# Kernel tuning notes

Measured on AMD Instinct MI355X. Metric: run time of the kernel, lower is better.

Reference implementation:

```python
import jax, jax.numpy as jnp
import numpy as np

B, N, D, H, F = 2, 2048, 1024, 16, 4096
HD = D // H


def setup_inputs() -> dict:
    key = jax.random.key(0)
    ks = jax.random.split(key, 16)
    s = 0.02
    x = jax.random.normal(ks[0], (B, N, D), jnp.float32)
    # tail padding: lengths in [N//2, N]; position >= length is padded
    lengths = jax.random.randint(ks[1], (B,), N // 2, N + 1)
    key_padding_mask = jnp.arange(N)[None, :] >= lengths[:, None]  # [B,N] bool, True = pad
    return {
        "x": x,
        "key_padding_mask": key_padding_mask,
        "ln1_g": jnp.ones((D,), jnp.float32),
        "ln1_b": jnp.zeros((D,), jnp.float32),
        "w_in": jax.random.normal(ks[2], (3 * D, D), jnp.float32) * s,  # packed QKV in_proj
        "b_in": jnp.zeros((3 * D,), jnp.float32),
        "w_out": jax.random.normal(ks[3], (D, D), jnp.float32) * s,
        "b_out": jnp.zeros((D,), jnp.float32),
        "ln2_g": jnp.ones((D,), jnp.float32),
        "ln2_b": jnp.zeros((D,), jnp.float32),
        "w1": jax.random.normal(ks[4], (F, D), jnp.float32) * s,
        "b1": jnp.zeros((F,), jnp.float32),
        "w2": jax.random.normal(ks[5], (D, F), jnp.float32) * s,
        "b2": jnp.zeros((D,), jnp.float32),
    }


def _layernorm(x, g, b):
    # source LayerNorm forces fp32 then casts back
    xf = x.astype(jnp.float32)
    m = xf.mean(-1, keepdims=True)
    v = xf.var(-1, keepdims=True)
    return (((xf - m) * jax.lax.rsqrt(v + 1e-5)) * g + b).astype(x.dtype)


def _quick_gelu(x):
    return x * jax.nn.sigmoid(1.702 * x)


def _block(x, key_padding_mask, ln1_g, ln1_b, w_in, b_in, w_out, b_out,
           ln2_g, ln2_b, w1, b1, w2, b2):
    n = x.shape[1]
    # combined mask: causal OR key-pad, with diagonal unmasked for padded query rows
    causal = jnp.triu(jnp.ones((n, n), bool), 1)                      # [N,N]
    combined = causal[None] | key_padding_mask[:, None, :]            # [B,N,N]
    diag = jnp.eye(n, dtype=bool)
    combined = combined & ~(diag[None] & key_padding_mask[:, :, None])

    # --- attention (pre-norm) ---
    xn = _layernorm(x, ln1_g, ln1_b)
    qkv = xn @ w_in.T + b_in                                          # [B,N,3D]
    q, k, v = jnp.split(qkv, 3, axis=-1)
    def heads(t):
        return t.reshape(x.shape[0], n, H, HD).transpose(0, 2, 1, 3)  # [B,H,N,hd]
    q, k, v = heads(q), heads(k), heads(v)
    scores = jnp.einsum('bhqd,bhkd->bhqk', q, k) / np.sqrt(HD)        # [B,H,N,N]
    scores = jnp.where(combined[:, None], -jnp.inf, scores)
    probs = jax.nn.softmax(scores, axis=-1)                           # [B,H,N,N]
    attn = jnp.einsum('bhqk,bhkd->bqhd', probs, v).reshape(x.shape[0], n, D)
    attn = attn @ w_out.T + b_out
    attn = jnp.where(key_padding_mask[:, :, None], 0.0, attn)         # zero padded queries
    weights = probs.mean(axis=1)                                      # need_weights avg over heads

    x = x + attn
    # --- FFN (pre-norm) ---
    xn = _layernorm(x, ln2_g, ln2_b)
    mlp = _quick_gelu(xn @ w1.T + b1) @ w2.T + b2
    x = x + mlp
    return x, weights


def reference(x, key_padding_mask, ln1_g, ln1_b, w_in, b_in, w_out, b_out,
              ln2_g, ln2_b, w1, b1, w2, b2):
    return _block(x, key_padding_mask, ln1_g, ln1_b, w_in, b_in, w_out, b_out,
                  ln2_g, ln2_b, w1, b1, w2, b2)
```

## Files before the change

kernel.cpp:

```cpp
#include <hip/hip_runtime.h>
#include <hip/hip_bf16.h>
#include <stdint.h>

#define DEVI __device__ __forceinline__

typedef __attribute__((ext_vector_type(8)))  short bf16x8;
typedef __attribute__((ext_vector_type(4)))  short s16x4;
typedef __attribute__((ext_vector_type(4)))  float f32x4;
typedef __attribute__((ext_vector_type(16))) float f32x16;
typedef __attribute__((ext_vector_type(2)))  unsigned int u32x2;
typedef __attribute__((ext_vector_type(4)))  unsigned int u32x4;

#define L2E 1.44269504088896f

DEVI unsigned short f2bf(float f){
  union{float f; unsigned int u;} v; v.f = f;
  unsigned int u = v.u;
  u = u + 0x7FFFu + ((u >> 16) & 1u);
  return (unsigned short)(u >> 16);
}

DEVI unsigned int cvt_pk_bf16(float lo, float hi){
  unsigned int r;
  asm("v_cvt_pk_bf16_f32 %0, %1, %2" : "=v"(r) : "v"(lo), "v"(hi));
  return r;
}

typedef const __attribute__((address_space(1))) unsigned int gq_t;
typedef __attribute__((address_space(3))) unsigned int lq_t;

DEVI void gl_lds16(const unsigned short* g, unsigned short* l){
  __builtin_amdgcn_global_load_lds((gq_t*)(uintptr_t)g, (lq_t*)(uintptr_t)l, 16, 0, 0);
}

__global__ void prep_len(const unsigned char* mask, int* lens){
  __shared__ int nz, cnt0, cnt1;
  int tid = threadIdx.x;
  if(tid == 0){ nz = 0; cnt0 = 0; cnt1 = 0; }
  __syncthreads();
  int loc = 0;
  for(int i = tid; i < 4096; i += 256) loc |= mask[i];
  if(loc) atomicOr(&nz, 1);
  __syncthreads();
  bool isu8 = (nz != 0);
  const int* m32 = (const int*)mask;
  int c0 = 0, c1 = 0;
  for(int i = tid; i < 2048; i += 256){
    int p0 = isu8 ? (int)mask[i]        : m32[i];
    int p1 = isu8 ? (int)mask[2048 + i] : m32[2048 + i];
    c0 += (p0 == 0);
    c1 += (p1 == 0);
  }
  atomicAdd(&cnt0, c0);
  atomicAdd(&cnt1, c1);
  __syncthreads();
  if(tid == 0){ lens[0] = cnt0; lens[1] = cnt1; }
}

__global__ void conv_bf16(const float* s, unsigned short* d, int n4){
  int i = blockIdx.x * 256 + threadIdx.x;
  if(i >= n4) return;
  f32x4 v = *(const f32x4*)(s + (size_t)i*4);
  s16x4 o;
  o[0]=(short)f2bf(v[0]); o[1]=(short)f2bf(v[1]);
  o[2]=(short)f2bf(v[2]); o[3]=(short)f2bf(v[3]);
  *(s16x4*)(d + (size_t)i*4) = o;
}

__global__ __launch_bounds__(256)
void ln_k(const float* x, const float* g, const float* b, unsigned short* y){
  int row = blockIdx.x, tid = threadIdx.x;
  const float* xr = x + (size_t)row*1024;
  f32x4 v = *(const f32x4*)(xr + tid*4);
  float s = v[0]+v[1]+v[2]+v[3];
#pragma unroll
  for(int o=1;o<64;o<<=1) s += __shfl_xor(s, o, 64);
  __shared__ float red[8];
  if((tid & 63) == 0) red[tid>>6] = s;
  __syncthreads();
  float mean = (red[0]+red[1]+red[2]+red[3]) * 0.0009765625f;
  float d0=v[0]-mean, d1=v[1]-mean, d2=v[2]-mean, d3=v[3]-mean;
  float s2 = d0*d0 + d1*d1 + d2*d2 + d3*d3;
#pragma unroll
  for(int o=1;o<64;o<<=1) s2 += __shfl_xor(s2, o, 64);
  if((tid & 63) == 0) red[4 + (tid>>6)] = s2;
  __syncthreads();
  float var = (red[4]+red[5]+red[6]+red[7]) * 0.0009765625f;
  float rstd = rsqrtf(var + 1e-5f);
  f32x4 gg = *(const f32x4*)(g + tid*4);
  f32x4 bb = *(const f32x4*)(b + tid*4);
  s16x4 o;
  o[0] = (short)f2bf(d0*rstd*gg[0] + bb[0]);
  o[1] = (short)f2bf(d1*rstd*gg[1] + bb[1]);
  o[2] = (short)f2bf(d2*rstd*gg[2] + bb[2]);
  o[3] = (short)f2bf(d3*rstd*gg[3] + bb[3]);
  *(s16x4*)(y + (size_t)row*1024 + tid*4) = o;
}

struct GemmP {
  const unsigned short* Wt;
  const unsigned short* Xa;
  int Nmat, K;
  const float* bias;
  const float* resid;
  const int* lens;
  float* outF;
  unsigned short* outB;
};

template<int EPI, int NB>
__global__ __launch_bounds__(256)
void gemm_k(GemmP p){
  constexpr int NF = NB/32;
  __shared__ unsigned short lw[NB*64];
  __shared__ unsigned short lx[128*64];
  int nbn = p.Nmat / NB;
  int id = blockIdx.x;
  int cpx = gridDim.x >> 3;
  id = (id & 7)*cpx + (id >> 3);
  int bm = id / nbn, bn = id % nbn;
  int tid = threadIdx.x, lane = tid & 63, g = lane >> 4, l15 = lane & 15;
  int wave = tid >> 6, wm = wave & 1, wn = wave >> 1;

  const unsigned short* srcW[NB/32]; const unsigned short* srcX[4];
  unsigned short* dstW[NB/32]; unsigned short* dstX[4];
#pragma unroll
  for(int i=0;i<NB/32;++i){
    int slot = i*256 + tid, row = slot >> 3, c = slot & 7, cs = c ^ (row & 7);
    srcW[i] = p.Wt + (size_t)(bn*NB + row)*p.K + cs*8;
    dstW[i] = lw + (i*256 + (tid & 192))*8;
  }
#pragma unroll
  for(int i=0;i<4;++i){
    int slot = i*256 + tid, row = slot >> 3, c = slot & 7, cs = c ^ (row & 7);
    srcX[i] = p.Xa + (size_t)(bm*128 + row)*p.K + cs*8;
    dstX[i] = lx + (i*256 + (tid & 192))*8;
  }

  f32x4 acc[NF][4];
#pragma unroll
  for(int a=0;a<NF;++a)
#pragma unroll
    for(int bb=0;bb<4;++bb)
#pragma unroll
      for(int e=0;e<4;++e) acc[a][bb][e] = 0.f;

  int iters = p.K >> 6;
  for(int kt=0; kt<iters; ++kt){
#pragma unroll
    for(int i=0;i<NB/32;++i){
      gl_lds16(srcW[i], dstW[i]);
      srcW[i] += 64;
    }
#pragma unroll
    for(int i=0;i<4;++i){
      gl_lds16(srcX[i], dstX[i]);
      srcX[i] += 64;
    }
    __syncthreads();
#pragma unroll
    for(int kc=0;kc<2;++kc){
      bf16x8 af[NF], bfr[4];
#pragma unroll
      for(int nf=0;nf<NF;++nf){
        int row = wn*(16*NF) + nf*16 + l15;
        int ch = (kc*4 + g) ^ (row & 7);
        af[nf] = *(const bf16x8*)(lw + row*64 + ch*8);
      }
#pragma unroll
      for(int mf=0;mf<4;++mf){
        int row = wm*64 + mf*16 + l15;
        int ch = (kc*4 + g) ^ (row & 7);
        bfr[mf] = *(const bf16x8*)(lx + row*64 + ch*8);
      }
#pragma unroll
      for(int nf=0;nf<NF;++nf)
#pragma unroll
        for(int mf=0;mf<4;++mf)
          acc[nf][mf] = __builtin_amdgcn_mfma_f32_16x16x32_bf16(af[nf], bfr[mf], acc[nf][mf], 0, 0, 0);
    }
    __syncthreads();
  }

#pragma unroll
  for(int mf=0;mf<4;++mf){
    int m = bm*128 + wm*64 + mf*16 + l15;
#pragma unroll
    for(int nf=0;nf<NF;++nf){
      int n = bn*NB + wn*(16*NF) + nf*16 + g*4;
      f32x4 v = acc[nf][mf];
      f32x4 bz = *(const f32x4*)(p.bias + n);
      v = v + bz;
      if constexpr(EPI == 0){
        float sc = (n < 1024) ? 0.125f : 1.0f;
        s16x4 o;
#pragma unroll
        for(int e=0;e<4;++e) o[e] = (short)f2bf(v[e]*sc);
        *(s16x4*)(p.outB + (size_t)m*p.Nmat + n) = o;
      } else if constexpr(EPI == 1){
        int b_ = m >> 11, q = m & 2047;
        f32x4 r = *(const f32x4*)(p.resid + (size_t)m*1024 + n);
        if(q >= p.lens[b_]){ v[0]=0.f; v[1]=0.f; v[2]=0.f; v[3]=0.f; }
        v = v + r;
        *(f32x4*)(p.outF + (size_t)m*p.Nmat + n) = v;
      } else if constexpr(EPI == 2){
        s16x4 o;
#pragma unroll
        for(int e=0;e<4;++e){
          float sg = v[e]*__builtin_amdgcn_rcpf(1.f + exp2f(-1.702f*L2E*v[e]));
          o[e] = (short)f2bf(sg);
        }
        *(s16x4*)(p.outB + (size_t)m*p.Nmat + n) = o;
      } else {
        f32x4 r = *(const f32x4*)(p.resid + (size_t)m*p.Nmat + n);
        v = v + r;
        *(f32x4*)(p.outF + (size_t)m*p.Nmat + n) = v;
      }
    }
  }
}

__global__ __launch_bounds__(256)
void repack_vt(const unsigned short* qkv, unsigned short* vt){
  __shared__ unsigned short t[64*80];
  int id = blockIdx.x;
  int bh = id >> 5, nt = id & 31;
  int b = bh >> 4, h = bh & 15;
  int tid = threadIdx.x;
  int r = tid >> 2, c0 = (tid & 3)*16;
  const unsigned short* src = qkv + ((size_t)(b*2048 + nt*64 + r)*3072 + 2048 + h*64 + c0);
  bf16x8 v0 = *(const bf16x8*)(src);
  bf16x8 v1 = *(const bf16x8*)(src + 8);
  *(bf16x8*)(t + r*80 + c0) = v0;
  *(bf16x8*)(t + r*80 + c0 + 8) = v1;
  __syncthreads();
#pragma unroll
  for(int cc=0; cc<2; ++cc){
    int ci = cc*256 + tid;
    int hd = ci >> 3, nc = (ci & 7)*8;
    bf16x8 o;
#pragma unroll
    for(int i=0;i<8;++i) o[i] = (short)t[(nc+i)*80 + hd];
    *(bf16x8*)(vt + ((size_t)(bh*64 + hd)*2048 + nt*64 + nc)) = o;
  }
}

__global__ __launch_bounds__(256)
void attn_flash(const unsigned short* qkv, const unsigned short* vt,
                unsigned short* attnO, float* mrow, float* lrow, const int* lens)
{
  __shared__ unsigned short lk[2][64*64];
  __shared__ unsigned short lv[2][64*64];
  int id = blockIdx.x;
  int jj = id & 255;
  int bh = jj & 31;
  int qt = (id < 256) ? (15 - (jj >> 5)) : (jj >> 5);
  int b = bh >> 4, h = bh & 15;
  int tid = threadIdx.x, lane = tid & 63, wave = tid >> 6;
  int hi = lane >> 5, l31 = lane & 31;
  int q = qt*128 + wave*32 + l31;
  int len_b = lens[b];

  const unsigned short* qptr = qkv + ((size_t)(b*2048 + q)*3072 + h*64);
  bf16x8 qf[4];
#pragma unroll
  for(int ks=0;ks<4;++ks) qf[ks] = *(const bf16x8*)(qptr + ks*16 + hi*8);

  const unsigned short* srcK[2]; const unsigned short* srcV[2];
  int dof[2];
#pragma unroll
  for(int i=0;i<2;++i){
    int slot = i*256 + tid, row = slot >> 3, c = slot & 7, cs = c ^ (row & 7);
    srcK[i] = qkv + ((size_t)(b*2048 + row)*3072 + 1024 + h*64) + cs*8;
    srcV[i] = vt + ((size_t)(bh*64 + row)*2048) + cs*8;
    dof[i] = (i*256 + (tid & 192))*8;
  }

  f32x16 oacc[2];
#pragma unroll
  for(int a=0;a<2;++a)
#pragma unroll
    for(int e=0;e<16;++e) oacc[a][e] = 0.f;
  float mcur = -1e30f, lsum = 0.f;
  int ktmax = qt*2 + 1;

#pragma unroll
  for(int i=0;i<2;++i){
    gl_lds16(srcK[i], &lk[0][dof[i]]);
    gl_lds16(srcV[i], &lv[0][dof[i]]);
    srcK[i] += (size_t)64*3072;
    srcV[i] += 64;
  }
  __syncthreads();

  int buf = 0;
  for(int kt=0; kt<=ktmax; ++kt){
    if(kt < ktmax){
#pragma unroll
      for(int i=0;i<2;++i){
        gl_lds16(srcK[i], &lk[buf^1][dof[i]]);
        gl_lds16(srcV[i], &lv[buf^1][dof[i]]);
        srcK[i] += (size_t)64*3072;
        srcV[i] += 64;
      }
    }

    f32x16 s2[2];
#pragma unroll
    for(int kb=0;kb<2;++kb){
      f32x16 a;
#pragma unroll
      for(int e=0;e<16;++e) a[e] = 0.f;
      int row = kb*32 + l31;
#pragma unroll
      for(int ks=0;ks<4;++ks){
        int ch = (ks*2 + hi) ^ (row & 7);
        bf16x8 kf = *(const bf16x8*)(&lk[buf][0] + row*64 + ch*8);
        a = __builtin_amdgcn_mfma_f32_32x32x16_bf16(kf, qf[ks], a, 0, 0, 0);
      }
      s2[kb] = a;
    }

    float tmax = -1e30f;
    bool full = (kt*64 + 63 < qt*128 + wave*32) && (kt*64 + 64 <= len_b);
    if(full){
#pragma unroll
      for(int kb=0;kb<2;++kb)
#pragma unroll
        for(int r=0;r<16;++r){
          float tv = s2[kb][r]*L2E;
          s2[kb][r] = tv;
          tmax = fmaxf(tmax, tv);
        }
    } else {
#pragma unroll
      for(int kb=0;kb<2;++kb)
#pragma unroll
        for(int r=0;r<16;++r){
          int key = kt*64 + kb*32 + (r&3) + 8*(r>>2) + 4*hi;
          bool ok = (key == q) || ((key < q) && (key < len_b));
          float tv = ok ? s2[kb][r]*L2E : -1e30f;
          s2[kb][r] = tv;
          tmax = fmaxf(tmax, tv);
        }
    }
    tmax = fmaxf(tmax, __shfl_xor(tmax, 32, 64));

    if(!__all(tmax <= mcur + 8.f)){
      float mnew = fmaxf(mcur, tmax);
      float fsc = exp2f(mcur - mnew);
      lsum *= fsc;
#pragma unroll
      for(int a=0;a<2;++a)
#pragma unroll
        for(int e=0;e<16;++e) oacc[a][e] *= fsc;
      mcur = mnew;
    }
    float rsum = 0.f;
#pragma unroll
    for(int kb=0;kb<2;++kb)
#pragma unroll
      for(int r=0;r<16;++r){
        float pv = exp2f(s2[kb][r] - mcur);
        s2[kb][r] = pv;
        rsum += pv;
      }
    rsum += __shfl_xor(rsum, 32, 64);
    lsum += rsum;

#pragma unroll
    for(int ks=0;ks<4;++ks){
      int kb = ks >> 1, r0 = (ks & 1)*8;
      unsigned int a0 = cvt_pk_bf16(s2[kb][r0+0], s2[kb][r0+1]);
      unsigned int a1 = cvt_pk_bf16(s2[kb][r0+2], s2[kb][r0+3]);
      unsigned int a2 = cvt_pk_bf16(s2[kb][r0+4], s2[kb][r0+5]);
      unsigned int a3 = cvt_pk_bf16(s2[kb][r0+6], s2[kb][r0+7]);
      unsigned int b0 = __shfl_xor(a0, 32, 64);
      unsigned int b1 = __shfl_xor(a1, 32, 64);
      unsigned int b2 = __shfl_xor(a2, 32, 64);
      unsigned int b3 = __shfl_xor(a3, 32, 64);
      union { u32x4 u; bf16x8 s8; } pw;
      pw.u[0] = hi ? b2 : a0;
      pw.u[1] = hi ? b3 : a1;
      pw.u[2] = hi ? a2 : b0;
      pw.u[3] = hi ? a3 : b1;
#pragma unroll
      for(int af=0;af<2;++af){
        int vrow = af*32 + l31;
        int ch = (ks*2 + hi) ^ (vrow & 7);
        bf16x8 vf = *(const bf16x8*)(&lv[buf][0] + vrow*64 + ch*8);
        oacc[af] = __builtin_amdgcn_mfma_f32_32x32x16_bf16(vf, pw.s8, oacc[af], 0, 0, 0);
      }
    }
    __syncthreads();
    buf ^= 1;
  }

  float rl = __builtin_amdgcn_rcpf(lsum);
  if(hi == 0){
    mrow[(size_t)bh*2048 + q] = mcur;
    lrow[(size_t)bh*2048 + q] = lsum;
  }
  unsigned short* obase = attnO + ((size_t)(b*2048 + q)*1024 + h*64);
#pragma unroll
  for(int af=0;af<2;++af)
#pragma unroll
    for(int grp=0; grp<4; ++grp){
      int hd0 = af*32 + grp*8 + hi*4;
      u32x2 st;
      st[0] = cvt_pk_bf16(oacc[af][grp*4+0]*rl, oacc[af][grp*4+1]*rl);
      st[1] = cvt_pk_bf16(oacc[af][grp*4+2]*rl, oacc[af][grp*4+3]*rl);
      *(u32x2*)(obase + hd0) = st;
    }
}

__global__ void prep_c(const float* mrow, const float* lrow, float* cbuf){
  int i = blockIdx.x*256 + threadIdx.x;
  cbuf[i] = exp2f(-mrow[i]) * __builtin_amdgcn_rcpf(lrow[i]);
}

__global__ __launch_bounds__(256)
void attn_weights(const unsigned short* qkv, const float* cbuf,
                  float* wout, const int* lens)
{
  int id = blockIdx.x;
  int kt = id & 15, qt = (id >> 4) & 15, b = id >> 8;
  int tid = threadIdx.x;
  float* wtile = wout + ((size_t)(b*2048 + qt*128))*2048 + kt*128;

  if(kt > qt){
    f32x4 z; z[0]=0.f; z[1]=0.f; z[2]=0.f; z[3]=0.f;
#pragma unroll
    for(int i=0;i<8;++i){
      float* p = wtile + (size_t)(i*16 + (tid>>4))*2048 + (tid&15)*8;
      *(f32x4*)p = z; *(f32x4*)(p+4) = z;
    }
    return;
  }

  __shared__ unsigned short lk[2][128*64];
  __shared__ unsigned short lq[2][128*64];
  int lane = tid & 63, wave = tid >> 6, hi = lane >> 5, l31 = lane & 31;
  int len_b = lens[b];
  int q_abs = qt*128 + wave*32 + l31;

  const float* cb = cbuf + (size_t)(b*16)*2048 + q_abs;
  float ccs[16];
#pragma unroll
  for(int h=0;h<16;++h) ccs[h] = cb[(size_t)h*2048];

  const unsigned short* srcK[4]; const unsigned short* srcQ[4]; int dA[4];
#pragma unroll
  for(int i=0;i<4;++i){
    int d = i*256 + tid, row = d >> 3, c = d & 7, cs = c ^ (row & 7);
    srcK[i] = qkv + ((size_t)(b*2048 + kt*128 + row)*3072 + 1024) + cs*8;
    srcQ[i] = qkv + ((size_t)(b*2048 + qt*128 + row)*3072) + cs*8;
    dA[i] = d*8;
  }

  float wacc[4][16];
#pragma unroll
  for(int ksub=0;ksub<4;++ksub)
#pragma unroll
    for(int r=0;r<16;++r) wacc[ksub][r] = 0.f;

#pragma unroll
  for(int i=0;i<4;++i){
    gl_lds16(srcK[i], &lk[0][dA[i]]);
    gl_lds16(srcQ[i], &lq[0][dA[i]]);
  }
  __syncthreads();

  int buf = 0;
  for(int h=0;h<16;++h){
    if(h < 15){
#pragma unroll
      for(int i=0;i<4;++i){
        gl_lds16(srcK[i] + (h+1)*64, &lk[buf^1][dA[i]]);
        gl_lds16(srcQ[i] + (h+1)*64, &lq[buf^1][dA[i]]);
      }
    }
    bf16x8 qf[4];
#pragma unroll
    for(int ks=0;ks<4;++ks){
      int row = wave*32 + l31;
      int ch = (ks*2 + hi) ^ (row & 7);
      qf[ks] = *(const bf16x8*)(&lq[buf][0] + row*64 + ch*8);
    }
    float cc = ccs[h];
#pragma unroll
    for(int ksub=0;ksub<4;++ksub){
      f32x16 sc;
#pragma unroll
      for(int e=0;e<16;++e) sc[e] = 0.f;
#pragma unroll
      for(int ks=0;ks<4;++ks){
        int row = ksub*32 + l31;
        int ch = (ks*2 + hi) ^ (row & 7);
        bf16x8 kf = *(const bf16x8*)(&lk[buf][0] + row*64 + ch*8);
        sc = __builtin_amdgcn_mfma_f32_32x32x16_bf16(kf, qf[ks], sc, 0, 0, 0);
      }
#pragma unroll
      for(int r=0;r<16;++r)
        wacc[ksub][r] += exp2f(sc[r]*L2E) * cc;
    }
    __syncthreads();
    buf ^= 1;
  }

#pragma unroll
  for(int ksub=0;ksub<4;++ksub)
#pragma unroll
    for(int rg=0;rg<4;++rg){
      f32x4 v;
#pragma unroll
      for(int e=0;e<4;++e){
        int key_abs = kt*128 + ksub*32 + rg*8 + hi*4 + e;
        bool ok = (key_abs == q_abs) || ((key_abs < q_abs) && (key_abs < len_b));
        v[e] = ok ? wacc[ksub][rg*4 + e]*0.0625f : 0.f;
      }
      *(f32x4*)(wtile + (size_t)(wave*32 + l31)*2048 + ksub*32 + rg*8 + hi*4) = v;
    }
}

extern "C" void kernel_launch(void* const* d_in, const int* in_sizes, int n_in,
                              void* d_out, int out_size, void* d_ws, size_t ws_size,
                              hipStream_t stream)
{
  const float* x     = (const float*)d_in[0];
  const unsigned char* mask = (const unsigned char*)d_in[1];
  const float* ln1g  = (const float*)d_in[2];
  const float* ln1b  = (const float*)d_in[3];
  const float* w_in  = (const float*)d_in[4];
  const float* b_in  = (const float*)d_in[5];
  const float* w_out = (const float*)d_in[6];
  const float* b_out = (const float*)d_in[7];
  const float* ln2g  = (const float*)d_in[8];
  const float* ln2b  = (const float*)d_in[9];
  const float* w1    = (const float*)d_in[10];
  const float* b1    = (const float*)d_in[11];
  const float* w2    = (const float*)d_in[12];
  const float* b2    = (const float*)d_in[13];
  float* out = (float*)d_out;

  char* ws = (char*)d_ws;
  size_t off = 0;
  auto take = [&](size_t bytes)->char*{
    char* p = ws + off; off += (bytes + 255) & ~(size_t)255; return p;
  };
  int* lens            = (int*)take(256);
  unsigned short* wq   = (unsigned short*)take((size_t)3072*1024*2);
  unsigned short* wo   = (unsigned short*)take((size_t)1024*1024*2);
  unsigned short* w1c  = (unsigned short*)take((size_t)4096*1024*2);
  unsigned short* w2c  = (unsigned short*)take((size_t)1024*4096*2);
  unsigned short* xn   = (unsigned short*)take((size_t)4096*1024*2);
  unsigned short* qkv  = (unsigned short*)take((size_t)4096*3072*2);
  unsigned short* vt   = (unsigned short*)take((size_t)32*64*2048*2);
  float* mrow          = (float*)take((size_t)32*2048*4);
  float* lrow          = (float*)take((size_t)32*2048*4);
  float* cbuf          = (float*)take((size_t)32*2048*4);
  unsigned short* aO   = (unsigned short*)take((size_t)4096*1024*2);
  float* x1            = (float*)take((size_t)4096*1024*4);
  unsigned short* hmid = (unsigned short*)take((size_t)4096*4096*2);

  prep_len<<<1,256,0,stream>>>(mask, lens);
  conv_bf16<<<3072,256,0,stream>>>(w_in, wq, 786432);
  conv_bf16<<<1024,256,0,stream>>>(w_out, wo, 262144);
  conv_bf16<<<4096,256,0,stream>>>(w1, w1c, 1048576);
  conv_bf16<<<4096,256,0,stream>>>(w2, w2c, 1048576);
  ln_k<<<4096,256,0,stream>>>(x, ln1g, ln1b, xn);

  GemmP p1{wq, xn, 3072, 1024, b_in, nullptr, nullptr, nullptr, qkv};
  gemm_k<0,128><<<768,256,0,stream>>>(p1);
  repack_vt<<<1024,256,0,stream>>>(qkv, vt);
  attn_flash<<<512,256,0,stream>>>(qkv, vt, aO, mrow, lrow, lens);
  prep_c<<<256,256,0,stream>>>(mrow, lrow, cbuf);
  attn_weights<<<512,256,0,stream>>>(qkv, cbuf, out + 4194304, lens);

  GemmP p2{wo, aO, 1024, 1024, b_out, x, lens, x1, nullptr};
  gemm_k<1,64><<<512,256,0,stream>>>(p2);
  ln_k<<<4096,256,0,stream>>>(x1, ln2g, ln2b, xn);
  GemmP p3{w1c, xn, 4096, 1024, b1, nullptr, nullptr, nullptr, hmid};
  gemm_k<2,128><<<1024,256,0,stream>>>(p3);
  GemmP p4{w2c, hmid, 1024, 4096, b2, x1, nullptr, out, nullptr};
  gemm_k<3,64><<<512,256,0,stream>>>(p4);
}
```

Measured before the change: 338.1 us.

## Triple-buffer attention K/V loads, fold log2e into Q, widen GEMM K-tile

The flash-attention loop moves from double to triple LDS buffering. The two per-iteration __syncthreads are replaced by one explicit vmcnt wait plus a barrier, and MFMA sections get raised wave priority, so global loads overlap compute with fewer stalls. The log2(e) factor is folded into the Q scaling in the QKV GEMM epilogue, which removes a multiply per score in both attention kernels; rounding of Q to bf16 now includes that factor. The GEMM is templated on its K-tile depth, and the two 64-wide-N GEMMs use K=128 to halve loop iterations and barriers, at the cost of more shared memory per block.

```diff
diff --git a/kernel.cpp b/kernel.cpp
--- a/kernel.cpp
+++ b/kernel.cpp
@@ -108,12 +108,15 @@
   unsigned short* outB;
 };
 
-template<int EPI, int NB>
+template<int EPI, int NB, int KB>
 __global__ __launch_bounds__(256)
 void gemm_k(GemmP p){
   constexpr int NF = NB/32;
-  __shared__ unsigned short lw[NB*64];
-  __shared__ unsigned short lx[128*64];
+  constexpr int CPR = KB/8;
+  constexpr int NW = (NB*KB)/2048;
+  constexpr int NX = (128*KB)/2048;
+  __shared__ unsigned short lw[NB*KB];
+  __shared__ unsigned short lx[128*KB];
   int nbn = p.Nmat / NB;
   int id = blockIdx.x;
   int cpx = gridDim.x >> 3;
@@ -122,17 +125,17 @@
   int tid = threadIdx.x, lane = tid & 63, g = lane >> 4, l15 = lane & 15;
   int wave = tid >> 6, wm = wave & 1, wn = wave >> 1;
 
-  const unsigned short* srcW[NB/32]; const unsigned short* srcX[4];
-  unsigned short* dstW[NB/32]; unsigned short* dstX[4];
-#pragma unroll
-  for(int i=0;i<NB/32;++i){
-    int slot = i*256 + tid, row = slot >> 3, c = slot & 7, cs = c ^ (row & 7);
+  const unsigned short* srcW[NW]; const unsigned short* srcX[NX];
+  unsigned short* dstW[NW]; unsigned short* dstX[NX];
+#pragma unroll
+  for(int i=0;i<NW;++i){
+    int slot = i*256 + tid, row = slot/CPR, c = slot%CPR, cs = c ^ (row & 7);
     srcW[i] = p.Wt + (size_t)(bn*NB + row)*p.K + cs*8;
     dstW[i] = lw + (i*256 + (tid & 192))*8;
   }
 #pragma unroll
-  for(int i=0;i<4;++i){
-    int slot = i*256 + tid, row = slot >> 3, c = slot & 7, cs = c ^ (row & 7);
+  for(int i=0;i<NX;++i){
+    int slot = i*256 + tid, row = slot/CPR, c = slot%CPR, cs = c ^ (row & 7);
     srcX[i] = p.Xa + (size_t)(bm*128 + row)*p.K + cs*8;
     dstX[i] = lx + (i*256 + (tid & 192))*8;
   }
@@ -145,33 +148,33 @@
 #pragma unroll
       for(int e=0;e<4;++e) acc[a][bb][e] = 0.f;
 
-  int iters = p.K >> 6;
+  int iters = p.K / KB;
   for(int kt=0; kt<iters; ++kt){
 #pragma unroll
-    for(int i=0;i<NB/32;++i){
+    for(int i=0;i<NW;++i){
       gl_lds16(srcW[i], dstW[i]);
-      srcW[i] += 64;
-    }
-#pragma unroll
-    for(int i=0;i<4;++i){
+      srcW[i] += KB;
+    }
+#pragma unroll
+    for(int i=0;i<NX;++i){
       gl_lds16(srcX[i], dstX[i]);
-      srcX[i] += 64;
+      srcX[i] += KB;
     }
     __syncthreads();
 #pragma unroll
-    for(int kc=0;kc<2;++kc){
+    for(int kc=0;kc<KB/32;++kc){
       bf16x8 af[NF], bfr[4];
 #pragma unroll
       for(int nf=0;nf<NF;++nf){
         int row = wn*(16*NF) + nf*16 + l15;
         int ch = (kc*4 + g) ^ (row & 7);
-        af[nf] = *(const bf16x8*)(lw + row*64 + ch*8);
+        af[nf] = *(const bf16x8*)(lw + row*KB + ch*8);
       }
 #pragma unroll
       for(int mf=0;mf<4;++mf){
         int row = wm*64 + mf*16 + l15;
         int ch = (kc*4 + g) ^ (row & 7);
-        bfr[mf] = *(const bf16x8*)(lx + row*64 + ch*8);
+        bfr[mf] = *(const bf16x8*)(lx + row*KB + ch*8);
       }
 #pragma unroll
       for(int nf=0;nf<NF;++nf)
@@ -192,7 +195,7 @@
       f32x4 bz = *(const f32x4*)(p.bias + n);
       v = v + bz;
       if constexpr(EPI == 0){
-        float sc = (n < 1024) ? 0.125f : 1.0f;
+        float sc = (n < 1024) ? 0.125f*L2E : 1.0f;
         s16x4 o;
 #pragma unroll
         for(int e=0;e<4;++e) o[e] = (short)f2bf(v[e]*sc);
@@ -249,8 +252,8 @@
 void attn_flash(const unsigned short* qkv, const unsigned short* vt,
                 unsigned short* attnO, float* mrow, float* lrow, const int* lens)
 {
-  __shared__ unsigned short lk[2][64*64];
-  __shared__ unsigned short lv[2][64*64];
+  __shared__ unsigned short lk[3][64*64];
+  __shared__ unsigned short lv[3][64*64];
   int id = blockIdx.x;
   int jj = id & 255;
   int bh = jj & 31;
@@ -265,6 +268,7 @@
   bf16x8 qf[4];
 #pragma unroll
   for(int ks=0;ks<4;++ks) qf[ks] = *(const bf16x8*)(qptr + ks*16 + hi*8);
+  asm volatile("" :: "v"(qf[0]), "v"(qf[1]), "v"(qf[2]), "v"(qf[3]), "s"(len_b));
 
   const unsigned short* srcK[2]; const unsigned short* srcV[2];
   int dof[2];
@@ -291,21 +295,26 @@
     srcK[i] += (size_t)64*3072;
     srcV[i] += 64;
   }
-  __syncthreads();
 
   int buf = 0;
   for(int kt=0; kt<=ktmax; ++kt){
+    int nb = buf + 1; if(nb == 3) nb = 0;
     if(kt < ktmax){
 #pragma unroll
       for(int i=0;i<2;++i){
-        gl_lds16(srcK[i], &lk[buf^1][dof[i]]);
-        gl_lds16(srcV[i], &lv[buf^1][dof[i]]);
+        gl_lds16(srcK[i], &lk[nb][dof[i]]);
+        gl_lds16(srcV[i], &lv[nb][dof[i]]);
         srcK[i] += (size_t)64*3072;
         srcV[i] += 64;
       }
-    }
+      asm volatile("s_waitcnt vmcnt(4)" ::: "memory");
+    } else {
+      asm volatile("s_waitcnt vmcnt(0)" ::: "memory");
+    }
+    asm volatile("s_barrier" ::: "memory");
 
     f32x16 s2[2];
+    __builtin_amdgcn_s_setprio(1);
 #pragma unroll
     for(int kb=0;kb<2;++kb){
       f32x16 a;
@@ -320,6 +329,7 @@
       }
       s2[kb] = a;
     }
+    __builtin_amdgcn_s_setprio(0);
 
     float tmax = -1e30f;
     bool full = (kt*64 + 63 < qt*128 + wave*32) && (kt*64 + 64 <= len_b);
@@ -327,11 +337,8 @@
 #pragma unroll
       for(int kb=0;kb<2;++kb)
 #pragma unroll
-        for(int r=0;r<16;++r){
-          float tv = s2[kb][r]*L2E;
-          s2[kb][r] = tv;
-          tmax = fmaxf(tmax, tv);
-        }
+        for(int r=0;r<16;++r)
+          tmax = fmaxf(tmax, s2[kb][r]);
     } else {
 #pragma unroll
       for(int kb=0;kb<2;++kb)
@@ -339,7 +346,7 @@
         for(int r=0;r<16;++r){
           int key = kt*64 + kb*32 + (r&3) + 8*(r>>2) + 4*hi;
           bool ok = (key == q) || ((key < q) && (key < len_b));
-          float tv = ok ? s2[kb][r]*L2E : -1e30f;
+          float tv = ok ? s2[kb][r] : -1e30f;
           s2[kb][r] = tv;
           tmax = fmaxf(tmax, tv);
         }
@@ -368,6 +375,7 @@
     rsum += __shfl_xor(rsum, 32, 64);
     lsum += rsum;
 
+    __builtin_amdgcn_s_setprio(1);
 #pragma unroll
     for(int ks=0;ks<4;++ks){
       int kb = ks >> 1, r0 = (ks & 1)*8;
@@ -392,8 +400,8 @@
         oacc[af] = __builtin_amdgcn_mfma_f32_32x32x16_bf16(vf, pw.s8, oacc[af], 0, 0, 0);
       }
     }
-    __syncthreads();
-    buf ^= 1;
+    __builtin_amdgcn_s_setprio(0);
+    buf = nb;
   }
 
   float rl = __builtin_amdgcn_rcpf(lsum);
@@ -502,7 +510,7 @@
       }
 #pragma unroll
       for(int r=0;r<16;++r)
-        wacc[ksub][r] += exp2f(sc[r]*L2E) * cc;
+        wacc[ksub][r] += exp2f(sc[r]) * cc;
     }
     __syncthreads();
     buf ^= 1;
@@ -571,17 +579,17 @@
   ln_k<<<4096,256,0,stream>>>(x, ln1g, ln1b, xn);
 
   GemmP p1{wq, xn, 3072, 1024, b_in, nullptr, nullptr, nullptr, qkv};
-  gemm_k<0,128><<<768,256,0,stream>>>(p1);
+  gemm_k<0,128,64><<<768,256,0,stream>>>(p1);
   repack_vt<<<1024,256,0,stream>>>(qkv, vt);
   attn_flash<<<512,256,0,stream>>>(qkv, vt, aO, mrow, lrow, lens);
   prep_c<<<256,256,0,stream>>>(mrow, lrow, cbuf);
   attn_weights<<<512,256,0,stream>>>(qkv, cbuf, out + 4194304, lens);
 
   GemmP p2{wo, aO, 1024, 1024, b_out, x, lens, x1, nullptr};
-  gemm_k<1,64><<<512,256,0,stream>>>(p2);
+  gemm_k<1,64,128><<<512,256,0,stream>>>(p2);
   ln_k<<<4096,256,0,stream>>>(x1, ln2g, ln2b, xn);
   GemmP p3{w1c, xn, 4096, 1024, b1, nullptr, nullptr, nullptr, hmid};
-  gemm_k<2,128><<<1024,256,0,stream>>>(p3);
+  gemm_k<2,128,64><<<1024,256,0,stream>>>(p3);
   GemmP p4{w2c, hmid, 1024, 4096, b2, x1, nullptr, out, nullptr};
-  gemm_k<3,64><<<512,256,0,stream>>>(p4);
-}
+  gemm_k<3,64,128><<<512,256,0,stream>>>(p4);
+}
```

After: 323.8 us. 4.2% less time.
